# Kernel optimization log

Hardware: AMD Instinct MI355X
Metric: run time of the kernel (lower is better)

Reference implementation:

```python
import jax, jax.numpy as jnp
import numpy as np


def setup_inputs() -> dict:
    key = jax.random.key(0)
    ks = jax.random.split(key, 7)
    B, T, H = 8192, 4096, 10
    s = 1.0 / np.sqrt(H)  # torch nn.RNN/Linear init scale
    return {
        "x": jax.random.normal(ks[0], (B, T), dtype=jnp.float32),
        "W_ih": jax.random.uniform(ks[1], (H, 1), jnp.float32, -s, s),
        "W_hh": jax.random.uniform(ks[2], (H, H), jnp.float32, -s, s),
        "b_ih": jax.random.uniform(ks[3], (H,), jnp.float32, -s, s),
        "b_hh": jax.random.uniform(ks[4], (H,), jnp.float32, -s, s),
        "fc_W": jax.random.uniform(ks[5], (1, H), jnp.float32, -s, s),
        "fc_b": jax.random.uniform(ks[6], (1,), jnp.float32, -s, s),
    }


def reference(x, W_ih, W_hh, b_ih, b_hh, fc_W, fc_b):
    # x: [B, T] -> unsqueeze(-1) gives input_size=1, so per-step input term is
    # x_t * W_ih[:, 0]  (outer product of [B] scalar inputs with the [H] column).
    B, T = x.shape
    H = W_hh.shape[0]
    bias = b_ih + b_hh  # [H]
    w_in = W_ih[:, 0]   # [H]
    xs = x.T            # [T, B] scan over time

    def step(h, x_t):
        # h: [B, H], x_t: [B]
        h_new = jnp.tanh(x_t[:, None] * w_in[None, :] + h @ W_hh.T + bias)
        return h_new, None

    h0 = jnp.zeros((B, H), dtype=x.dtype)
    h_last, _ = jax.lax.scan(step, h0, xs)
    # fc on last timestep's hidden state: [B, H] @ [H, 1] + [1]
    return h_last @ fc_W.T + fc_b
```

## Files before the change

kernel.cpp:

```cpp
#include <hip/hip_runtime.h>
#include <stdint.h>


#define H 10

typedef __fp16 h2 __attribute__((ext_vector_type(2)));
typedef __fp16 h4 __attribute__((ext_vector_type(4)));
typedef float  f4 __attribute__((ext_vector_type(4)));

#if __has_builtin(__builtin_amdgcn_exp2f)
__device__ __forceinline__ float fast_exp2(float x) { return __builtin_amdgcn_exp2f(x); }
#else
__device__ __forceinline__ float fast_exp2(float x) { return __exp2f(x); }
#endif

#if __has_builtin(__builtin_amdgcn_rcpf)
__device__ __forceinline__ float fast_rcp(float x) { return __builtin_amdgcn_rcpf(x); }
#else
__device__ __forceinline__ float fast_rcp(float x) { return 1.0f / x; }
#endif

#if __has_builtin(__builtin_amdgcn_cvt_pkrtz)
__device__ __forceinline__ h2 pk2(float a, float b) { return __builtin_amdgcn_cvt_pkrtz(a, b); }
#else
__device__ __forceinline__ h2 pk2(float a, float b) { h2 r; r.x = (__fp16)a; r.y = (__fp16)b; return r; }
#endif

struct hpair { h2 lo, hi; };
__device__ __forceinline__ h4 mk_h4(h2 lo, h2 hi) {
    hpair p; p.lo = lo; p.hi = hi;
    return __builtin_bit_cast(h4, p);
}

__device__ __forceinline__ f4 mfma_16x16x16f16(h4 a, h4 b, f4 c) {
#if defined(__HIP_DEVICE_COMPILE__)
    return __builtin_amdgcn_mfma_f32_16x16x16f16(a, b, c, 0, 0, 0);
#else
    return c;
#endif
}

#define RNN_STEP(XV)                                                          \
    do {                                                                      \
        f4 c;                                                                 \
        c[0] = __builtin_fmaf((XV), winp[0], biasc[0]);                       \
        c[1] = __builtin_fmaf((XV), winp[1], biasc[1]);                       \
        c[2] = __builtin_fmaf((XV), winp[2], biasc[2]);                       \
        c[3] = __builtin_fmaf((XV), winp[3], biasc[3]);                       \
        f4 d = mfma_16x16x16f16(m_frag, rb, c);                               \
        _Pragma("unroll")                                                     \
        for (int j = 0; j < 4; ++j) {                                         \
            float e = fast_exp2(d[j]);                                        \
            rf[j] = fast_rcp(e + 1.0f);                                       \
        }                                                                     \
        rb = mk_h4(pk2(rf[0], rf[1]), pk2(rf[2], rf[3]));                     \
    } while (0)

#define STEP8(V0, V1)                                                         \
    do {                                                                      \
        RNN_STEP((V0).x); RNN_STEP((V0).y); RNN_STEP((V0).z); RNN_STEP((V0).w); \
        RNN_STEP((V1).x); RNN_STEP((V1).y); RNN_STEP((V1).z); RNN_STEP((V1).w); \
    } while (0)

__global__ __launch_bounds__(64) void rnn_mfma_r(
    const float* __restrict__ x,
    const float* __restrict__ W_ih,
    const float* __restrict__ W_hh,
    const float* __restrict__ b_ih,
    const float* __restrict__ b_hh,
    const float* __restrict__ fc_W,
    const float* __restrict__ fc_b,
    float* __restrict__ out,
    int B, int T)
{
    const int l = threadIdx.x;
    const int n = l & 15;
    const int g = l >> 4;
    const int b = blockIdx.x * 16 + n;

    const float C = 2.8853900817779268f;

    h4 m_frag;
#pragma unroll
    for (int i = 0; i < 4; ++i) {
        const int k = 4 * g + i;
        const float w = (n < H && k < H) ? -2.0f * C * W_hh[n * H + k] : 0.0f;
        m_frag[i] = (__fp16)w;
    }

    float winp[4], biasc[4], fcw[4];
#pragma unroll
    for (int j = 0; j < 4; ++j) {
        const int u = 4 * g + j;
        const bool live = (u < H);
        float rowsum = 0.0f;
        if (live) {
#pragma unroll
            for (int k = 0; k < H; ++k) rowsum += W_hh[u * H + k];
        }
        winp[j]  = live ? C * W_ih[u] : 0.0f;
        biasc[j] = live ? C * (b_ih[u] + b_hh[u] + rowsum) : 0.0f;
        fcw[j]   = live ? fc_W[u] : 0.0f;
    }

    const __fp16 half16 = (__fp16)0.5f;
    h4 rb = {half16, half16, half16, half16};
    float rf[4] = {0.5f, 0.5f, 0.5f, 0.5f};

    const int brow = (b < B) ? b : (B - 1);
    const float* xr = x + (size_t)brow * (size_t)T;

    int t = 0;
    if (((T & 7) == 0) && T >= 24) {
        const int nb = T >> 3;
        float4 a0 = *(const float4*)(xr + 0);
        float4 a1 = *(const float4*)(xr + 4);
        float4 b0 = *(const float4*)(xr + 8);
        float4 b1 = *(const float4*)(xr + 12);
        for (int blk = 0; blk < nb - 2; ++blk) {
            const float* xf = xr + 8 * (blk + 2);
            float4 f0 = *(const float4*)(xf);
            float4 f1 = *(const float4*)(xf + 4);
            STEP8(a0, a1);
            a0 = b0; a1 = b1;
            b0 = f0; b1 = f1;
        }
        STEP8(a0, a1);
        STEP8(b0, b1);
        t = T;
    }
    for (; t < T; ++t) {
        float xq = xr[t];
        RNN_STEP(xq);
    }

    float acc = 0.0f;
#pragma unroll
    for (int j = 0; j < 4; ++j) {
        const float h = __builtin_fmaf(-2.0f, rf[j], 1.0f);
        acc = __builtin_fmaf(h, fcw[j], acc);
    }
    acc += __shfl_xor(acc, 16, 64);
    acc += __shfl_xor(acc, 32, 64);
    if (g == 0 && b < B) out[b] = acc + fc_b[0];
}

extern "C" void kernel_launch(void* const* d_in, const int* in_sizes, int n_in,
                              void* d_out, int out_size, void* d_ws, size_t ws_size,
                              hipStream_t stream) {
    const float* x    = (const float*)d_in[0];
    const float* W_ih = (const float*)d_in[1];
    const float* W_hh = (const float*)d_in[2];
    const float* b_ih = (const float*)d_in[3];
    const float* b_hh = (const float*)d_in[4];
    const float* fc_W = (const float*)d_in[5];
    const float* fc_b = (const float*)d_in[6];
    float* out = (float*)d_out;

    const int B = out_size;
    const int T = in_sizes[0] / B;

    const int blocks = (B + 15) / 16;
    rnn_mfma_r<<<blocks, 64, 0, stream>>>(x, W_ih, W_hh, b_ih, b_hh,
                                          fc_W, fc_b, out, B, T);
}
```

Baseline: 306.2 us.

## Fold input term into MFMA via permuted hidden layout and packed x operand

```diff
diff --git a/kernel.cpp b/kernel.cpp
--- a/kernel.cpp
+++ b/kernel.cpp
@@ -40,29 +40,23 @@
 #endif
 }
 
-#define RNN_STEP(XV)                                                          \
+#define RNN_STEP(XPK)                                                         \
     do {                                                                      \
-        f4 c;                                                                 \
-        c[0] = __builtin_fmaf((XV), winp[0], biasc[0]);                       \
-        c[1] = __builtin_fmaf((XV), winp[1], biasc[1]);                       \
-        c[2] = __builtin_fmaf((XV), winp[2], biasc[2]);                       \
-        c[3] = __builtin_fmaf((XV), winp[3], biasc[3]);                       \
-        f4 d = mfma_16x16x16f16(m_frag, rb, c);                               \
-        _Pragma("unroll")                                                     \
-        for (int j = 0; j < 4; ++j) {                                         \
-            float e = fast_exp2(d[j]);                                        \
-            rf[j] = fast_rcp(e + 1.0f);                                       \
-        }                                                                     \
-        rb = mk_h4(pk2(rf[0], rf[1]), pk2(rf[2], rf[3]));                     \
+        f4 d = mfma_16x16x16f16(m_frag, rb, biasc);                           \
+        float e0 = fast_exp2(d[0]);                                           \
+        float e1 = fast_exp2(d[1]);                                           \
+        float e2 = fast_exp2(d[2]);                                           \
+        rf0 = fast_rcp(e0 + 1.0f);                                            \
+        rf1 = fast_rcp(e1 + 1.0f);                                            \
+        rf2 = fast_rcp(e2 + 1.0f);                                            \
+        h2 lo = pk2(rf0, rf1);                                                \
+        h2 hi = pk2(rf2, rf2);                                                \
+        unsigned hiw = is_g3 ? __builtin_bit_cast(unsigned, (XPK))            \
+                             : __builtin_bit_cast(unsigned, hi);              \
+        rb = mk_h4(lo, __builtin_bit_cast(h2, hiw));                          \
     } while (0)
 
-#define STEP8(V0, V1)                                                         \
-    do {                                                                      \
-        RNN_STEP((V0).x); RNN_STEP((V0).y); RNN_STEP((V0).z); RNN_STEP((V0).w); \
-        RNN_STEP((V1).x); RNN_STEP((V1).y); RNN_STEP((V1).z); RNN_STEP((V1).w); \
-    } while (0)
-
-__global__ __launch_bounds__(64) void rnn_mfma_r(
+__global__ __launch_bounds__(64) void rnn_mfma_perm(
     const float* __restrict__ x,
     const float* __restrict__ W_ih,
     const float* __restrict__ W_hh,
@@ -77,35 +71,42 @@
     const int n = l & 15;
     const int g = l >> 4;
     const int b = blockIdx.x * 16 + n;
+    const bool is_g3 = (g == 3);
 
     const float C = 2.8853900817779268f;
 
+    const int uor[16] = {0, 4, 8, -1,  1, 5, 9, -1,  2, 6, -1, -1,  3, 7, -1, -1};
+
+    const int ur = uor[n];
     h4 m_frag;
 #pragma unroll
     for (int i = 0; i < 4; ++i) {
         const int k = 4 * g + i;
-        const float w = (n < H && k < H) ? -2.0f * C * W_hh[n * H + k] : 0.0f;
+        float w = 0.0f;
+        if (ur >= 0) {
+            if (k == 14)            w = C * W_ih[ur];
+            else if (uor[k] >= 0)   w = -2.0f * C * W_hh[ur * H + uor[k]];
+        }
         m_frag[i] = (__fp16)w;
     }
 
-    float winp[4], biasc[4], fcw[4];
+    f4 biasc;
+    float fcw[4];
 #pragma unroll
     for (int j = 0; j < 4; ++j) {
-        const int u = 4 * g + j;
-        const bool live = (u < H);
+        const int u = uor[4 * g + j];
         float rowsum = 0.0f;
-        if (live) {
+        if (u >= 0) {
 #pragma unroll
             for (int k = 0; k < H; ++k) rowsum += W_hh[u * H + k];
         }
-        winp[j]  = live ? C * W_ih[u] : 0.0f;
-        biasc[j] = live ? C * (b_ih[u] + b_hh[u] + rowsum) : 0.0f;
-        fcw[j]   = live ? fc_W[u] : 0.0f;
+        biasc[j] = (u >= 0) ? C * (b_ih[u] + b_hh[u] + rowsum) : 0.0f;
+        fcw[j]   = (u >= 0) ? fc_W[u] : 0.0f;
     }
 
-    const __fp16 half16 = (__fp16)0.5f;
-    h4 rb = {half16, half16, half16, half16};
-    float rf[4] = {0.5f, 0.5f, 0.5f, 0.5f};
+    float rf0 = 0.5f, rf1 = 0.5f, rf2 = 0.5f;
+    h2 halfpk = pk2(0.5f, 0.5f);
+    h4 rb;
 
     const int brow = (b < B) ? b : (B - 1);
     const float* xr = x + (size_t)brow * (size_t)T;
@@ -115,31 +116,50 @@
         const int nb = T >> 3;
         float4 a0 = *(const float4*)(xr + 0);
         float4 a1 = *(const float4*)(xr + 4);
+        rb = mk_h4(halfpk, is_g3 ? pk2(a0.x, 1.0f) : halfpk);
         float4 b0 = *(const float4*)(xr + 8);
         float4 b1 = *(const float4*)(xr + 12);
         for (int blk = 0; blk < nb - 2; ++blk) {
             const float* xf = xr + 8 * (blk + 2);
             float4 f0 = *(const float4*)(xf);
             float4 f1 = *(const float4*)(xf + 4);
-            STEP8(a0, a1);
+            h2 xp0 = pk2(a0.y, 1.0f), xp1 = pk2(a0.z, 1.0f);
+            h2 xp2 = pk2(a0.w, 1.0f), xp3 = pk2(a1.x, 1.0f);
+            h2 xp4 = pk2(a1.y, 1.0f), xp5 = pk2(a1.z, 1.0f);
+            h2 xp6 = pk2(a1.w, 1.0f), xp7 = pk2(b0.x, 1.0f);
+            RNN_STEP(xp0); RNN_STEP(xp1); RNN_STEP(xp2); RNN_STEP(xp3);
+            RNN_STEP(xp4); RNN_STEP(xp5); RNN_STEP(xp6); RNN_STEP(xp7);
             a0 = b0; a1 = b1;
             b0 = f0; b1 = f1;
         }
-        STEP8(a0, a1);
-        STEP8(b0, b1);
+        {
+            h2 xp0 = pk2(a0.y, 1.0f), xp1 = pk2(a0.z, 1.0f);
+            h2 xp2 = pk2(a0.w, 1.0f), xp3 = pk2(a1.x, 1.0f);
+            h2 xp4 = pk2(a1.y, 1.0f), xp5 = pk2(a1.z, 1.0f);
+            h2 xp6 = pk2(a1.w, 1.0f), xp7 = pk2(b0.x, 1.0f);
+            RNN_STEP(xp0); RNN_STEP(xp1); RNN_STEP(xp2); RNN_STEP(xp3);
+            RNN_STEP(xp4); RNN_STEP(xp5); RNN_STEP(xp6); RNN_STEP(xp7);
+            h2 yp0 = pk2(b0.y, 1.0f), yp1 = pk2(b0.z, 1.0f);
+            h2 yp2 = pk2(b0.w, 1.0f), yp3 = pk2(b1.x, 1.0f);
+            h2 yp4 = pk2(b1.y, 1.0f), yp5 = pk2(b1.z, 1.0f);
+            h2 yp6 = pk2(b1.w, 1.0f), yp7 = pk2(0.0f, 1.0f);
+            RNN_STEP(yp0); RNN_STEP(yp1); RNN_STEP(yp2); RNN_STEP(yp3);
+            RNN_STEP(yp4); RNN_STEP(yp5); RNN_STEP(yp6); RNN_STEP(yp7);
+        }
         t = T;
+    } else {
+        rb = mk_h4(halfpk, is_g3 ? pk2((T > 0) ? xr[0] : 0.0f, 1.0f) : halfpk);
     }
     for (; t < T; ++t) {
-        float xq = xr[t];
-        RNN_STEP(xq);
+        float xnext = (t + 1 < T) ? xr[t + 1] : 0.0f;
+        h2 xp = pk2(xnext, 1.0f);
+        RNN_STEP(xp);
     }
 
     float acc = 0.0f;
-#pragma unroll
-    for (int j = 0; j < 4; ++j) {
-        const float h = __builtin_fmaf(-2.0f, rf[j], 1.0f);
-        acc = __builtin_fmaf(h, fcw[j], acc);
-    }
+    acc = __builtin_fmaf(__builtin_fmaf(-2.0f, rf0, 1.0f), fcw[0], acc);
+    acc = __builtin_fmaf(__builtin_fmaf(-2.0f, rf1, 1.0f), fcw[1], acc);
+    acc = __builtin_fmaf(__builtin_fmaf(-2.0f, rf2, 1.0f), fcw[2], acc);
     acc += __shfl_xor(acc, 16, 64);
     acc += __shfl_xor(acc, 32, 64);
     if (g == 0 && b < B) out[b] = acc + fc_b[0];
@@ -161,6 +181,6 @@
     const int T = in_sizes[0] / B;
 
     const int blocks = (B + 15) / 16;
-    rnn_mfma_r<<<blocks, 64, 0, stream>>>(x, W_ih, W_hh, b_ih, b_hh,
-                                          fc_W, fc_b, out, B, T);
+    rnn_mfma_perm<<<blocks, 64, 0, stream>>>(x, W_ih, W_hh, b_ih, b_hh,
+                                             fc_W, fc_b, out, B, T);
 }
```

Result: faster. 253.7 us (-17.1%).
